# Performance work log

Hardware: AMD Instinct MI355X
Metric: run time of the kernel (lower is better)

## Reference

```python
import jax, jax.numpy as jnp
import numpy as np

C = 512
HEADS = 4
GROUPS = 32
EPS = 1e-6


def setup_inputs() -> dict:
    key = jax.random.key(0)
    ks = jax.random.split(key, 6)
    s = 1.0 / np.sqrt(C)
    return {
        "x": jax.random.normal(ks[0], (2, C, 64, 64), dtype=jnp.float32),
        "gn_scale": jnp.ones((C,), jnp.float32),
        "gn_bias": jnp.zeros((C,), jnp.float32),
        "wq": jax.random.normal(ks[1], (C, C), jnp.float32) * s,
        "bq": jnp.zeros((C,), jnp.float32),
        "wk": jax.random.normal(ks[2], (C, C), jnp.float32) * s,
        "bk": jnp.zeros((C,), jnp.float32),
        "wv": jax.random.normal(ks[3], (C, C), jnp.float32) * s,
        "bv": jnp.zeros((C,), jnp.float32),
        "wo": jax.random.normal(ks[4], (C, C), jnp.float32) * s,
        "bo": jnp.zeros((C,), jnp.float32),
    }


def group_norm(x, scale, bias):
    # x: [b, c, h, w]; GroupNorm with 32 groups, eps 1e-6, affine
    b, c, h, w = x.shape
    xg = x.reshape(b, GROUPS, c // GROUPS, h, w)
    mean = jnp.mean(xg, axis=(2, 3, 4), keepdims=True)
    var = jnp.var(xg, axis=(2, 3, 4), keepdims=True)
    xg = (xg - mean) * jax.lax.rsqrt(var + EPS)
    x = xg.reshape(b, c, h, w)
    return x * scale[None, :, None, None] + bias[None, :, None, None]


def conv1x1(x, w, b):
    # 1x1 conv == per-pixel linear: [b,c,h,w] x [o,c] -> [b,o,h,w]
    return jnp.einsum('bchw,oc->bohw', x, w) + b[None, :, None, None]


def reference(x, gn_scale, gn_bias, wq, bq, wk, bk, wv, bv, wo, bo):
    b, c, h, w = x.shape
    hc = c // HEADS
    n = h * w

    h_ = group_norm(x, gn_scale, gn_bias)
    q = conv1x1(h_, wq, bq).reshape(b, HEADS, hc, n)
    k = conv1x1(h_, wk, bk).reshape(b, HEADS, hc, n)
    v = conv1x1(h_, wv, bv).reshape(b, HEADS, hc, n)

    # NOTE: scale uses full channel count c (repo quirk), not head_channel
    scale = jnp.asarray(c, x.dtype) ** -0.5
    scores = jnp.einsum('bhcn,bhcm->bhnm', q, k) * scale  # [b,H,N,N]
    attn = jax.nn.softmax(scores, axis=-1)
    out = jnp.einsum('bhnm,bhcm->bhcn', attn, v)  # [b,H,hc,N]

    out = out.reshape(b, c, h, w)
    return x + conv1x1(out, wo, bo)
```

## Files before the change

kernel.cpp:

```cpp
#include <hip/hip_runtime.h>

typedef float    f32x4 __attribute__((ext_vector_type(4)));
typedef short    bf16x8 __attribute__((ext_vector_type(8)));
typedef unsigned short u16;
typedef u16      u16x4 __attribute__((ext_vector_type(4)));
typedef unsigned u32;
typedef u32      u32x4 __attribute__((ext_vector_type(4)));

#define MFMA16(a, b, c) __builtin_amdgcn_mfma_f32_16x16x32_bf16((a), (b), (c), 0, 0, 0)

#define CCH 512
#define NPIX 4096
#define NHEAD 4
#define HC 128
#define NSPLIT 2
#define KVCHUNK (NPIX / NSPLIT)
#define QK_SCALE 0.04419417382415922f
#define LOG2E 1.4426950408889634f

__device__ __forceinline__ u16 f2b(float f) {
  unsigned u = __builtin_bit_cast(unsigned, f);
  u += 0x7FFFu + ((u >> 16) & 1u);
  return (u16)(u >> 16);
}
__device__ __forceinline__ float b2f(u16 b) {
  return __builtin_bit_cast(float, ((unsigned)b) << 16);
}

__device__ __forceinline__ void gl_lds16(const u16* g, u16* l) {
  __builtin_amdgcn_global_load_lds((const __attribute__((address_space(1))) void*)g,
                                   (__attribute__((address_space(3))) void*)l, 16, 0, 0);
}

__global__ void prep_k(const float* __restrict__ w0, const float* __restrict__ w1,
                       const float* __restrict__ w2, const float* __restrict__ w3,
                       u16* __restrict__ dst,
                       const float* __restrict__ x, float* __restrict__ pstats) {
  int blk = blockIdx.x, t = threadIdx.x;
  if (blk < 1024) {
    int m = blk >> 8;
    const float* src = (m == 0) ? w0 : (m == 1) ? w1 : (m == 2) ? w2 : w3;
    int i = ((blk & 255) * 256 + t) * 4;
    f32x4 v = *(const f32x4*)(src + i);
    u16x4 o = { f2b(v[0]), f2b(v[1]), f2b(v[2]), f2b(v[3]) };
    *(u16x4*)(dst + (size_t)m * (CCH * CCH) + i) = o;
    return;
  }
  int sblk = blk - 1024;
  const f32x4* p = (const f32x4*)(x + (size_t)sblk * 4096);
  int wv = t >> 6, l = t & 63;
  float s = 0.f, ss = 0.f;
  #pragma unroll
  for (int i = t; i < 1024; i += 256) {
    f32x4 v = p[i];
    s  += v[0] + v[1] + v[2] + v[3];
    ss += v[0]*v[0] + v[1]*v[1] + v[2]*v[2] + v[3]*v[3];
  }
  #pragma unroll
  for (int d = 32; d; d >>= 1) { s += __shfl_down(s, d, 64); ss += __shfl_down(ss, d, 64); }
  __shared__ float red[8];
  if (l == 0) { red[wv*2] = s; red[wv*2+1] = ss; }
  __syncthreads();
  if (t == 0) {
    pstats[sblk*2]   = red[0] + red[2] + red[4] + red[6];
    pstats[sblk*2+1] = red[1] + red[3] + red[5] + red[7];
  }
}

__global__ void gn_norm_k(const float* __restrict__ x, const float* __restrict__ gns,
                          const float* __restrict__ gnb, const float* __restrict__ pstats,
                          u16* __restrict__ Ht) {
  int t = threadIdx.x;
  int ct = blockIdx.x * 64, nt = blockIdx.y * 64, b = blockIdx.z;
  int c0 = ct + (t & 15) * 4;
  int n0 = nt + (t >> 4) * 4;
  const float* xb = x + ((size_t)b * CCH + c0) * NPIX + n0;
  int g = b * 32 + (c0 >> 4);
  const f32x4* ps = (const f32x4*)(pstats + g * 32);
  float s = 0.f, ss = 0.f;
  #pragma unroll
  for (int j = 0; j < 8; ++j) {
    f32x4 v = ps[j];
    s  += v[0] + v[2];
    ss += v[1] + v[3];
  }
  float mean = s * (1.f/65536.f);
  float var  = ss * (1.f/65536.f) - mean*mean;
  float rstd = rsqrtf(var + 1e-6f);
  f32x4 rows[4];
  #pragma unroll
  for (int j = 0; j < 4; ++j) {
    f32x4 v = *(const f32x4*)(xb + (size_t)j * NPIX);
    float a  = rstd * gns[c0 + j];
    float bb = gnb[c0 + j] - mean * a;
    rows[j] = v * a + bb;
  }
  #pragma unroll
  for (int i = 0; i < 4; ++i) {
    u16x4 o = { f2b(rows[0][i]), f2b(rows[1][i]), f2b(rows[2][i]), f2b(rows[3][i]) };
    *(u16x4*)(Ht + ((size_t)b * NPIX + n0 + i) * CCH + c0) = o;
  }
}

template<int MODE>
__device__ __forceinline__ void gemm_body(const u16* __restrict__ A,
                                          const u16* __restrict__ B,
                                          const float* __restrict__ bias,
                                          const float* __restrict__ bias2,
                                          u16* __restrict__ outb,
                                          u16* __restrict__ outb2,
                                          float alpha,
                                          int bx, int by, int z,
                                          u16* As, u16* Bs) {
  const int t = threadIdx.x, l = t & 63, wv = t >> 6;
  const int l16 = l & 15, lq = l >> 4;
  const int mt = bx * 128, nt = by * 64;
  const u16* Ap = A + (size_t)mt * CCH;
  const u16* Bp = (MODE == 3) ? (B + (size_t)nt * CCH)
                              : (B + ((size_t)z * NPIX + nt) * CCH);
  const int wm = (wv >> 1) * 64, wn = (wv & 1) * 32;
  f32x4 acc[4][2] = {};

  #pragma unroll
  for (int j = 0; j < 2; ++j) {
    int idx = t + j * 256;
    int row = idx >> 2, kc = (idx & 3) * 8;
    gl_lds16(Ap + (size_t)row * CCH + kc, As + idx * 8);
  }
  {
    int row = t >> 2, kc = (t & 3) * 8;
    gl_lds16(Bp + (size_t)row * CCH + kc, Bs + t * 8);
  }
  asm volatile("s_waitcnt vmcnt(0)" ::: "memory");
  __syncthreads();

#define GEMM_BODY(CUR, K0, DOSTAGE)                                                   \
  {                                                                                   \
    if (DOSTAGE) {                                                                    \
      _Pragma("unroll")                                                               \
      for (int j = 0; j < 2; ++j) {                                                   \
        int idx = t + j * 256;                                                        \
        int row = idx >> 2, kc = (idx & 3) * 8;                                       \
        gl_lds16(Ap + (size_t)row * CCH + (K0) + 32 + kc, As + ((CUR) ^ 1) * 4096 + idx * 8); \
      }                                                                               \
      {                                                                               \
        int row = t >> 2, kc = (t & 3) * 8;                                           \
        gl_lds16(Bp + (size_t)row * CCH + (K0) + 32 + kc, Bs + ((CUR) ^ 1) * 2048 + t * 8); \
      }                                                                               \
    }                                                                                 \
    bf16x8 af[4], bfr[2];                                                             \
    _Pragma("unroll")                                                                 \
    for (int i = 0; i < 4; ++i)                                                       \
      af[i]  = *(const bf16x8*)(As + (CUR) * 4096 + (wm + i * 16 + l16) * 32 + lq * 8); \
    _Pragma("unroll")                                                                 \
    for (int i = 0; i < 2; ++i)                                                       \
      bfr[i] = *(const bf16x8*)(Bs + (CUR) * 2048 + (wn + i * 16 + l16) * 32 + lq * 8); \
    _Pragma("unroll")                                                                 \
    for (int mi = 0; mi < 4; ++mi)                                                    \
      _Pragma("unroll")                                                               \
      for (int ni = 0; ni < 2; ++ni)                                                  \
        acc[mi][ni] = MFMA16(af[mi], bfr[ni], acc[mi][ni]);                           \
    asm volatile("s_waitcnt vmcnt(0)" ::: "memory");                                  \
    __syncthreads();                                                                  \
  }

  for (int k0 = 0; k0 < CCH; k0 += 64) {
    GEMM_BODY(0, k0, true)
    GEMM_BODY(1, k0 + 32, (k0 + 64 < CCH))
  }
#undef GEMM_BODY

  #pragma unroll
  for (int mi = 0; mi < 4; ++mi)
    #pragma unroll
    for (int ni = 0; ni < 2; ++ni)
      #pragma unroll
      for (int r = 0; r < 4; ++r) {
        int grow = mt + wm + mi * 16 + lq * 4 + r;
        int gcol = nt + wn + ni * 16 + l16;
        float v = acc[mi][ni][r];
        if (MODE == 1) {
          outb[((size_t)z * CCH + grow) * NPIX + gcol] = f2b(v + bias[grow]);
        } else {
          if (gcol < 512)
            outb[(size_t)grow * CCH + gcol] = f2b((v + bias[gcol]) * alpha);
          else
            outb2[(size_t)grow * CCH + (gcol - 512)] = f2b(v + bias2[gcol - 512]);
        }
      }
}

__global__ __launch_bounds__(256) void qkv_k(const u16* __restrict__ Ht,
                                             const u16* __restrict__ wb,
                                             const float* __restrict__ bq,
                                             const float* __restrict__ bk,
                                             const float* __restrict__ bv,
                                             u16* __restrict__ Qt, u16* __restrict__ Kt,
                                             u16* __restrict__ Vc, float alpha) {
  __shared__ __align__(16) u16 As[2][4096];
  __shared__ __align__(16) u16 Bs[2][2048];
  int blk = blockIdx.x;
  if (blk < 1024) {
    gemm_body<3>(Ht, wb, bq, bk, Qt, Kt, alpha, blk >> 4, blk & 15, 0,
                 &As[0][0], &Bs[0][0]);
  } else {
    int r = blk - 1024;
    gemm_body<1>(wb + 2u * 262144u, Ht, bv, nullptr, Vc, nullptr, 1.0f,
                 r & 3, (r >> 2) & 63, r >> 8, &As[0][0], &Bs[0][0]);
  }
}

__global__ __launch_bounds__(256, 2) void flash_k(const u16* __restrict__ Qt,
                                                  const u16* __restrict__ Kt,
                                                  const u16* __restrict__ Vc,
                                                  u16* __restrict__ sl0, u16* __restrict__ sl1,
                                                  float* __restrict__ mlp) {
  __shared__ __align__(16) char lds[32768];
  const int t = threadIdx.x, wv = t >> 6, l = t & 63;
  const int l16 = l & 15, lq = l >> 4;
  const int orig = blockIdx.x;
  const int gid = (orig & 7) * 64 + (orig >> 3);
  const int qx = gid & 31, grp = gid >> 5;
  const int hd = grp & 3, b = (grp >> 2) & 1, s = grp >> 3;
  const int qt0 = qx * 128 + wv * 32;

  const u16* Q = Qt + ((size_t)b * NPIX + qt0) * CCH + hd * HC;
  const u16* Kbase = Kt + (size_t)b * NPIX * CCH + hd * HC;
  const u16* Vbase = Vc + (size_t)b * CCH * NPIX + (size_t)hd * HC * NPIX;
  u16* slab = (s == 0) ? sl0 : sl1;
  u16* Ob = slab + ((size_t)(b * NHEAD + hd) * NPIX + qt0) * HC;
  size_t mlR0 = (size_t)s * 32768 + (size_t)(b * NHEAD + hd) * NPIX + qt0;

  bf16x8 qf[2][4];
  #pragma unroll
  for (int mi = 0; mi < 2; ++mi)
    #pragma unroll
    for (int kk = 0; kk < 4; ++kk)
      qf[mi][kk] = *(const bf16x8*)(Q + (size_t)(mi * 16 + l16) * CCH + kk * 32 + lq * 8);

  const int m_beg = s * KVCHUNK;
  const int vb2 = (lq & 1) * 32 + (lq >> 1) * 16;

  int kbase[4];
  #pragma unroll
  for (int kk = 0; kk < 4; ++kk)
    kbase[kk] = l16 * 256 + ((kk * 64 + lq * 16) ^ ((l16 & 7) << 4));
  const int vbase = 16384 + l16 * 64 + (vb2 ^ ((l16 & 3) << 4));

  u32 kgo[2], vgo[2];
  #pragma unroll
  for (int j = 0; j < 2; ++j) {
    int g = j * 256 + t;
    { int row = g >> 4, src = ((g & 15) << 4) ^ ((row & 7) << 4);
      kgo[j] = (u32)row * CCH + (src >> 1); }
    { int row = g >> 2, src = ((g & 3) << 4) ^ ((row & 3) << 4);
      vgo[j] = (u32)row * NPIX + (src >> 1); }
  }

  const short one_bf = (short)0x3F80;
  const bf16x8 vones = { one_bf, one_bf, one_bf, one_bf, one_bf, one_bf, one_bf, one_bf };

  f32x4 oacc[2][8] = {};
  f32x4 osum[2] = {};

  {
    const u16* kg = Kbase + (size_t)m_beg * CCH;
    const u16* vg = Vbase + m_beg;
    #pragma unroll
    for (int j = 0; j < 2; ++j) {
      gl_lds16(kg + kgo[j], (u16*)lds + (j * 256 + t) * 8);
      gl_lds16(vg + vgo[j], (u16*)(lds + 16384) + (j * 256 + t) * 8);
    }
  }
  asm volatile("s_waitcnt vmcnt(0)" ::: "memory");
  __syncthreads();

  const int NT = KVCHUNK / 32;

#define FLASH_BODY(CUR, M0, DOSTAGE)                                                   \
  {                                                                                    \
    if (DOSTAGE) {                                                                     \
      const u16* kg = Kbase + (size_t)((M0) + 32) * CCH;                               \
      const u16* vg = Vbase + ((M0) + 32);                                             \
      _Pragma("unroll")                                                                \
      for (int j = 0; j < 2; ++j) {                                                    \
        gl_lds16(kg + kgo[j], (u16*)(lds + ((CUR) ^ 1) * 8192) + (j * 256 + t) * 8);   \
        gl_lds16(vg + vgo[j], (u16*)(lds + 16384 + ((CUR) ^ 1) * 8192) + (j * 256 + t) * 8); \
      }                                                                                \
    }                                                                                  \
    f32x4 S[2][2] = {};                                                                \
    __builtin_amdgcn_s_setprio(1);                                                     \
    _Pragma("unroll")                                                                  \
    for (int kk = 0; kk < 4; ++kk)                                                     \
      _Pragma("unroll")                                                                \
      for (int mm = 0; mm < 2; ++mm) {                                                 \
        bf16x8 kf = *(const bf16x8*)(lds + kbase[kk] + mm * 4096 + (CUR) * 8192);      \
        S[0][mm] = MFMA16(kf, qf[0][kk], S[0][mm]);                                    \
        S[1][mm] = MFMA16(kf, qf[1][kk], S[1][mm]);                                    \
      }                                                                                \
    __builtin_amdgcn_s_setprio(0);                                                     \
    u32 pk[2][2][2];                                                                   \
    _Pragma("unroll")                                                                  \
    for (int mi = 0; mi < 2; ++mi) {                                                   \
      _Pragma("unroll")                                                                \
      for (int mm = 0; mm < 2; ++mm) {                                                 \
        f32x4 p;                                                                       \
        _Pragma("unroll")                                                              \
        for (int r = 0; r < 4; ++r) p[r] = exp2f(S[mi][mm][r]);                        \
        asm("v_cvt_pk_bf16_f32 %0, %1, %2" : "=v"(pk[mi][mm][0]) : "v"(p[0]), "v"(p[1])); \
        asm("v_cvt_pk_bf16_f32 %0, %1, %2" : "=v"(pk[mi][mm][1]) : "v"(p[2]), "v"(p[3])); \
      }                                                                                \
    }                                                                                  \
    bf16x8 pa[2];                                                                      \
    _Pragma("unroll")                                                                  \
    for (int mi = 0; mi < 2; ++mi) {                                                   \
      u32 a0 = pk[mi][0][0], a1 = pk[mi][0][1];                                        \
      u32 b0 = pk[mi][1][0], b1 = pk[mi][1][1];                                        \
      asm("v_permlane16_swap_b32 %0, %1" : "+v"(a0), "+v"(b0));                        \
      asm("v_permlane16_swap_b32 %0, %1" : "+v"(a1), "+v"(b1));                        \
      u32x4 w = { a0, a1, b0, b1 };                                                    \
      pa[mi] = __builtin_bit_cast(bf16x8, w);                                          \
    }                                                                                  \
    __builtin_amdgcn_s_setprio(1);                                                     \
    osum[0] = MFMA16(pa[0], vones, osum[0]);                                           \
    osum[1] = MFMA16(pa[1], vones, osum[1]);                                           \
    _Pragma("unroll")                                                                  \
    for (int cc = 0; cc < 8; ++cc) {                                                   \
      bf16x8 vf = *(const bf16x8*)(lds + vbase + cc * 1024 + (CUR) * 8192);            \
      oacc[0][cc] = MFMA16(pa[0], vf, oacc[0][cc]);                                    \
      oacc[1][cc] = MFMA16(pa[1], vf, oacc[1][cc]);                                    \
    }                                                                                  \
    __builtin_amdgcn_s_setprio(0);                                                     \
    asm volatile("s_waitcnt vmcnt(0)" ::: "memory");                                   \
    __syncthreads();                                                                   \
  }

  for (int it = 0; it < NT; it += 2) {
    FLASH_BODY(0, m_beg + it * 32, true)
    FLASH_BODY(1, m_beg + it * 32 + 32, (it + 2 < NT))
  }
#undef FLASH_BODY

  #pragma unroll
  for (int mi = 0; mi < 2; ++mi)
    #pragma unroll
    for (int cc = 0; cc < 8; ++cc)
      #pragma unroll
      for (int r = 0; r < 4; ++r)
        Ob[(size_t)(mi * 16 + lq * 4 + r) * HC + cc * 16 + l16] = f2b(oacc[mi][cc][r]);
  if (l16 == 0) {
    #pragma unroll
    for (int mi = 0; mi < 2; ++mi)
      #pragma unroll
      for (int r = 0; r < 4; ++r)
        mlp[mlR0 + mi * 16 + lq * 4 + r] = osum[mi][r];
  }
}

__global__ __launch_bounds__(256) void fgemm_k(const u16* __restrict__ Wo,
                                               const u16* __restrict__ sl0,
                                               const u16* __restrict__ sl1,
                                               const float* __restrict__ ml,
                                               const float* __restrict__ bias,
                                               const float* __restrict__ resid,
                                               float* __restrict__ outf) {
  __shared__ __align__(16) u16 As[2][4096];
  __shared__ __align__(16) u16 B0[2][2048];
  __shared__ __align__(16) u16 B1[2][2048];
  const int t = threadIdx.x, l = t & 63, wv = t >> 6;
  const int l16 = l & 15, lq = l >> 4;
  const int mt = blockIdx.x * 128, nt = blockIdx.y * 64, z = blockIdx.z;
  const u16* Ap = Wo + (size_t)mt * CCH;
  const int wm = (wv >> 1) * 64, wn = (wv & 1) * 32;

  float lsum[4][2];
  #pragma unroll
  for (int h = 0; h < 4; ++h)
    #pragma unroll
    for (int ni = 0; ni < 2; ++ni) {
      int gcol = nt + wn + ni * 16 + l16;
      int R = ((z * 4 + h) << 12) + gcol;
      lsum[h][ni] = ml[R] + ml[32768 + R];
    }

  f32x4 acc[4][2] = {};

  #pragma unroll
  for (int j = 0; j < 2; ++j) {
    int idx = t + j * 256;
    int row = idx >> 2, kc = (idx & 3) * 8;
    gl_lds16(Ap + (size_t)row * CCH + kc, &As[0][0] + idx * 8);
  }
  {
    int row = t >> 2, kc = (t & 3) * 8;
    size_t srow = ((size_t)(z * 4) * NPIX + nt + row) * HC + kc;
    gl_lds16(sl0 + srow, &B0[0][0] + t * 8);
    gl_lds16(sl1 + srow, &B1[0][0] + t * 8);
  }
  asm volatile("s_waitcnt vmcnt(0)" ::: "memory");
  __syncthreads();

#define FG_BODY(CUR, K0, DOSTAGE)                                                     \
  {                                                                                   \
    if (DOSTAGE) {                                                                    \
      const int kn = (K0) + 32;                                                       \
      const int hn = kn >> 7, cn = kn & 127;                                          \
      _Pragma("unroll")                                                               \
      for (int j = 0; j < 2; ++j) {                                                   \
        int idx = t + j * 256;                                                        \
        int row = idx >> 2, kc = (idx & 3) * 8;                                       \
        gl_lds16(Ap + (size_t)row * CCH + kn + kc, &As[(CUR) ^ 1][0] + idx * 8);      \
      }                                                                               \
      {                                                                               \
        int row = t >> 2, kc = (t & 3) * 8;                                           \
        size_t srow = ((size_t)(z * 4 + hn) * NPIX + nt + row) * HC + cn + kc;        \
        gl_lds16(sl0 + srow, &B0[(CUR) ^ 1][0] + t * 8);                              \
        gl_lds16(sl1 + srow, &B1[(CUR) ^ 1][0] + t * 8);                              \
      }                                                                               \
    }                                                                                 \
    bf16x8 af[4], b0f[2], b1f[2];                                                     \
    _Pragma("unroll")                                                                 \
    for (int i = 0; i < 4; ++i)                                                       \
      af[i]  = *(const bf16x8*)(&As[CUR][0] + (wm + i * 16 + l16) * 32 + lq * 8);     \
    _Pragma("unroll")                                                                 \
    for (int i = 0; i < 2; ++i) {                                                     \
      b0f[i] = *(const bf16x8*)(&B0[CUR][0] + (wn + i * 16 + l16) * 32 + lq * 8);     \
      b1f[i] = *(const bf16x8*)(&B1[CUR][0] + (wn + i * 16 + l16) * 32 + lq * 8);     \
    }                                                                                 \
    _Pragma("unroll")                                                                 \
    for (int mi = 0; mi < 4; ++mi)                                                    \
      _Pragma("unroll")                                                               \
      for (int ni = 0; ni < 2; ++ni) {                                                \
        acc[mi][ni] = MFMA16(af[mi], b0f[ni], acc[mi][ni]);                           \
        acc[mi][ni] = MFMA16(af[mi], b1f[ni], acc[mi][ni]);                           \
      }                                                                               \
    asm volatile("s_waitcnt vmcnt(0)" ::: "memory");                                  \
    __syncthreads();                                                                  \
  }

  #pragma unroll
  for (int h = 0; h < 4; ++h) {
    if (h) {
      #pragma unroll
      for (int ni = 0; ni < 2; ++ni) {
        float rat = lsum[h][ni] / lsum[h - 1][ni];
        #pragma unroll
        for (int mi = 0; mi < 4; ++mi) acc[mi][ni] *= rat;
      }
    }
    FG_BODY(0, h * 128,      true)
    FG_BODY(1, h * 128 + 32, true)
    FG_BODY(0, h * 128 + 64, true)
    FG_BODY(1, h * 128 + 96, (h < 3))
  }
#undef FG_BODY

  #pragma unroll
  for (int ni = 0; ni < 2; ++ni) {
    float inv3 = 1.f / lsum[3][ni];
    int gcol = nt + wn + ni * 16 + l16;
    #pragma unroll
    for (int mi = 0; mi < 4; ++mi)
      #pragma unroll
      for (int r = 0; r < 4; ++r) {
        int grow = mt + wm + mi * 16 + lq * 4 + r;
        size_t off = ((size_t)z * CCH + grow) * NPIX + gcol;
        outf[off] = acc[mi][ni][r] * inv3 + bias[grow] + resid[off];
      }
  }
}

extern "C" void kernel_launch(void* const* d_in, const int* in_sizes, int n_in,
                              void* d_out, int out_size, void* d_ws, size_t ws_size,
                              hipStream_t stream) {
  const float* x   = (const float*)d_in[0];
  const float* gns = (const float*)d_in[1];
  const float* gnb = (const float*)d_in[2];
  const float* wq  = (const float*)d_in[3];
  const float* bq  = (const float*)d_in[4];
  const float* wk  = (const float*)d_in[5];
  const float* bk  = (const float*)d_in[6];
  const float* wv  = (const float*)d_in[7];
  const float* bv  = (const float*)d_in[8];
  const float* wo  = (const float*)d_in[9];
  const float* bo  = (const float*)d_in[10];
  float* out = (float*)d_out;
  char* ws = (char*)d_ws;

  u16*   wb    = (u16*)ws;
  u16*   Ht    = (u16*)(ws + (size_t)( 2u << 20));
  u16*   Qt    = (u16*)(ws + (size_t)(10u << 20));
  u16*   Kt    = (u16*)(ws + (size_t)(18u << 20));
  u16*   Vc    = (u16*)(ws + (size_t)(26u << 20));
  u16*   sl1   = (u16*)(ws + (size_t)(34u << 20));
  float* mlb   = (float*)(ws + (size_t)(42u << 20));
  float* stats = (float*)(ws + (size_t)(43u << 20));
  u16*   sl0   = Ht;

  prep_k    <<<dim3(2048, 1, 1), 256, 0, stream>>>(wq, wk, wv, wo, wb, x, stats);
  gn_norm_k <<<dim3(8, 64, 2),   256, 0, stream>>>(x, gns, gnb, stats, Ht);
  qkv_k     <<<dim3(1536, 1, 1), 256, 0, stream>>>(Ht, wb, bq, bk, bv, Qt, Kt, Vc,
                                                   QK_SCALE * LOG2E);
  flash_k   <<<dim3(512, 1, 1),  256, 0, stream>>>(Qt, Kt, Vc, sl0, sl1, mlb);
  fgemm_k   <<<dim3(4, 64, 2),   256, 0, stream>>>(wb + 3u * 262144u, sl0, sl1, mlb,
                                                   bo, x, out);
}
```

Before: 147.9 us.

## Enlarge QKV GEMM tiles and split flash attention KV range three ways

```diff
diff --git a/kernel.cpp b/kernel.cpp
--- a/kernel.cpp
+++ b/kernel.cpp
@@ -13,8 +13,6 @@
 #define NPIX 4096
 #define NHEAD 4
 #define HC 128
-#define NSPLIT 2
-#define KVCHUNK (NPIX / NSPLIT)
 #define QK_SCALE 0.04419417382415922f
 #define LOG2E 1.4426950408889634f
 
@@ -114,22 +112,19 @@
                                           u16* As, u16* Bs) {
   const int t = threadIdx.x, l = t & 63, wv = t >> 6;
   const int l16 = l & 15, lq = l >> 4;
-  const int mt = bx * 128, nt = by * 64;
+  const int mt = bx * 128, nt = by * 128;
   const u16* Ap = A + (size_t)mt * CCH;
   const u16* Bp = (MODE == 3) ? (B + (size_t)nt * CCH)
                               : (B + ((size_t)z * NPIX + nt) * CCH);
-  const int wm = (wv >> 1) * 64, wn = (wv & 1) * 32;
-  f32x4 acc[4][2] = {};
+  const int wm = (wv >> 1) * 64, wn = (wv & 1) * 64;
+  f32x4 acc[4][4] = {};
 
   #pragma unroll
   for (int j = 0; j < 2; ++j) {
     int idx = t + j * 256;
     int row = idx >> 2, kc = (idx & 3) * 8;
     gl_lds16(Ap + (size_t)row * CCH + kc, As + idx * 8);
-  }
-  {
-    int row = t >> 2, kc = (t & 3) * 8;
-    gl_lds16(Bp + (size_t)row * CCH + kc, Bs + t * 8);
+    gl_lds16(Bp + (size_t)row * CCH + kc, Bs + idx * 8);
   }
   asm volatile("s_waitcnt vmcnt(0)" ::: "memory");
   __syncthreads();
@@ -142,23 +137,19 @@
         int idx = t + j * 256;                                                        \
         int row = idx >> 2, kc = (idx & 3) * 8;                                       \
         gl_lds16(Ap + (size_t)row * CCH + (K0) + 32 + kc, As + ((CUR) ^ 1) * 4096 + idx * 8); \
-      }                                                                               \
-      {                                                                               \
-        int row = t >> 2, kc = (t & 3) * 8;                                           \
-        gl_lds16(Bp + (size_t)row * CCH + (K0) + 32 + kc, Bs + ((CUR) ^ 1) * 2048 + t * 8); \
+        gl_lds16(Bp + (size_t)row * CCH + (K0) + 32 + kc, Bs + ((CUR) ^ 1) * 4096 + idx * 8); \
       }                                                                               \
     }                                                                                 \
-    bf16x8 af[4], bfr[2];                                                             \
+    bf16x8 af[4], bfr[4];                                                             \
     _Pragma("unroll")                                                                 \
-    for (int i = 0; i < 4; ++i)                                                       \
+    for (int i = 0; i < 4; ++i) {                                                     \
       af[i]  = *(const bf16x8*)(As + (CUR) * 4096 + (wm + i * 16 + l16) * 32 + lq * 8); \
-    _Pragma("unroll")                                                                 \
-    for (int i = 0; i < 2; ++i)                                                       \
-      bfr[i] = *(const bf16x8*)(Bs + (CUR) * 2048 + (wn + i * 16 + l16) * 32 + lq * 8); \
+      bfr[i] = *(const bf16x8*)(Bs + (CUR) * 4096 + (wn + i * 16 + l16) * 32 + lq * 8); \
+    }                                                                                 \
     _Pragma("unroll")                                                                 \
     for (int mi = 0; mi < 4; ++mi)                                                    \
       _Pragma("unroll")                                                               \
-      for (int ni = 0; ni < 2; ++ni)                                                  \
+      for (int ni = 0; ni < 4; ++ni)                                                  \
         acc[mi][ni] = MFMA16(af[mi], bfr[ni], acc[mi][ni]);                           \
     asm volatile("s_waitcnt vmcnt(0)" ::: "memory");                                  \
     __syncthreads();                                                                  \
@@ -173,7 +164,7 @@
   #pragma unroll
   for (int mi = 0; mi < 4; ++mi)
     #pragma unroll
-    for (int ni = 0; ni < 2; ++ni)
+    for (int ni = 0; ni < 4; ++ni)
       #pragma unroll
       for (int r = 0; r < 4; ++r) {
         int grow = mt + wm + mi * 16 + lq * 4 + r;
@@ -198,15 +189,15 @@
                                              u16* __restrict__ Qt, u16* __restrict__ Kt,
                                              u16* __restrict__ Vc, float alpha) {
   __shared__ __align__(16) u16 As[2][4096];
-  __shared__ __align__(16) u16 Bs[2][2048];
+  __shared__ __align__(16) u16 Bs[2][4096];
   int blk = blockIdx.x;
-  if (blk < 1024) {
-    gemm_body<3>(Ht, wb, bq, bk, Qt, Kt, alpha, blk >> 4, blk & 15, 0,
+  if (blk < 512) {
+    gemm_body<3>(Ht, wb, bq, bk, Qt, Kt, alpha, blk & 63, blk >> 6, 0,
                  &As[0][0], &Bs[0][0]);
   } else {
-    int r = blk - 1024;
+    int r = blk - 512;
     gemm_body<1>(wb + 2u * 262144u, Ht, bv, nullptr, Vc, nullptr, 1.0f,
-                 r & 3, (r >> 2) & 63, r >> 8, &As[0][0], &Bs[0][0]);
+                 r & 3, (r >> 2) & 31, r >> 7, &As[0][0], &Bs[0][0]);
   }
 }
 
@@ -214,12 +205,13 @@
                                                   const u16* __restrict__ Kt,
                                                   const u16* __restrict__ Vc,
                                                   u16* __restrict__ sl0, u16* __restrict__ sl1,
+                                                  u16* __restrict__ sl2,
                                                   float* __restrict__ mlp) {
   __shared__ __align__(16) char lds[32768];
   const int t = threadIdx.x, wv = t >> 6, l = t & 63;
   const int l16 = l & 15, lq = l >> 4;
   const int orig = blockIdx.x;
-  const int gid = (orig & 7) * 64 + (orig >> 3);
+  const int gid = (orig & 7) * 96 + (orig >> 3);
   const int qx = gid & 31, grp = gid >> 5;
   const int hd = grp & 3, b = (grp >> 2) & 1, s = grp >> 3;
   const int qt0 = qx * 128 + wv * 32;
@@ -227,7 +219,7 @@
   const u16* Q = Qt + ((size_t)b * NPIX + qt0) * CCH + hd * HC;
   const u16* Kbase = Kt + (size_t)b * NPIX * CCH + hd * HC;
   const u16* Vbase = Vc + (size_t)b * CCH * NPIX + (size_t)hd * HC * NPIX;
-  u16* slab = (s == 0) ? sl0 : sl1;
+  u16* slab = (s == 0) ? sl0 : (s == 1) ? sl1 : sl2;
   u16* Ob = slab + ((size_t)(b * NHEAD + hd) * NPIX + qt0) * HC;
   size_t mlR0 = (size_t)s * 32768 + (size_t)(b * NHEAD + hd) * NPIX + qt0;
 
@@ -238,7 +230,8 @@
     for (int kk = 0; kk < 4; ++kk)
       qf[mi][kk] = *(const bf16x8*)(Q + (size_t)(mi * 16 + l16) * CCH + kk * 32 + lq * 8);
 
-  const int m_beg = s * KVCHUNK;
+  const int m_beg = (s == 0) ? 0 : (s == 1) ? 1376 : 2752;
+  const int NT    = (s == 2) ? 42 : 43;
   const int vb2 = (lq & 1) * 32 + (lq >> 1) * 16;
 
   int kbase[4];
@@ -274,8 +267,6 @@
   }
   asm volatile("s_waitcnt vmcnt(0)" ::: "memory");
   __syncthreads();
-
-  const int NT = KVCHUNK / 32;
 
 #define FLASH_BODY(CUR, M0, DOSTAGE)                                                   \
   {                                                                                    \
@@ -335,9 +326,13 @@
     __syncthreads();                                                                   \
   }
 
-  for (int it = 0; it < NT; it += 2) {
+  int it = 0;
+  for (; it + 2 <= NT; it += 2) {
     FLASH_BODY(0, m_beg + it * 32, true)
     FLASH_BODY(1, m_beg + it * 32 + 32, (it + 2 < NT))
+  }
+  if (NT & 1) {
+    FLASH_BODY(0, m_beg + (NT - 1) * 32, false)
   }
 #undef FLASH_BODY
 
@@ -360,6 +355,7 @@
 __global__ __launch_bounds__(256) void fgemm_k(const u16* __restrict__ Wo,
                                                const u16* __restrict__ sl0,
                                                const u16* __restrict__ sl1,
+                                               const u16* __restrict__ sl2,
                                                const float* __restrict__ ml,
                                                const float* __restrict__ bias,
                                                const float* __restrict__ resid,
@@ -367,6 +363,7 @@
   __shared__ __align__(16) u16 As[2][4096];
   __shared__ __align__(16) u16 B0[2][2048];
   __shared__ __align__(16) u16 B1[2][2048];
+  __shared__ __align__(16) u16 B2[2][2048];
   const int t = threadIdx.x, l = t & 63, wv = t >> 6;
   const int l16 = l & 15, lq = l >> 4;
   const int mt = blockIdx.x * 128, nt = blockIdx.y * 64, z = blockIdx.z;
@@ -380,7 +377,7 @@
     for (int ni = 0; ni < 2; ++ni) {
       int gcol = nt + wn + ni * 16 + l16;
       int R = ((z * 4 + h) << 12) + gcol;
-      lsum[h][ni] = ml[R] + ml[32768 + R];
+      lsum[h][ni] = ml[R] + ml[32768 + R] + ml[65536 + R];
     }
 
   f32x4 acc[4][2] = {};
@@ -396,6 +393,7 @@
     size_t srow = ((size_t)(z * 4) * NPIX + nt + row) * HC + kc;
     gl_lds16(sl0 + srow, &B0[0][0] + t * 8);
     gl_lds16(sl1 + srow, &B1[0][0] + t * 8);
+    gl_lds16(sl2 + srow, &B2[0][0] + t * 8);
   }
   asm volatile("s_waitcnt vmcnt(0)" ::: "memory");
   __syncthreads();
@@ -416,23 +414,26 @@
         size_t srow = ((size_t)(z * 4 + hn) * NPIX + nt + row) * HC + cn + kc;        \
         gl_lds16(sl0 + srow, &B0[(CUR) ^ 1][0] + t * 8);                              \
         gl_lds16(sl1 + srow, &B1[(CUR) ^ 1][0] + t * 8);                              \
+        gl_lds16(sl2 + srow, &B2[(CUR) ^ 1][0] + t * 8);                              \
       }                                                                               \
     }                                                                                 \
-    bf16x8 af[4], b0f[2], b1f[2];                                                     \
+    bf16x8 af[4], b0f[2], b1f[2], b2f_[2];                                            \
     _Pragma("unroll")                                                                 \
     for (int i = 0; i < 4; ++i)                                                       \
       af[i]  = *(const bf16x8*)(&As[CUR][0] + (wm + i * 16 + l16) * 32 + lq * 8);     \
     _Pragma("unroll")                                                                 \
     for (int i = 0; i < 2; ++i) {                                                     \
-      b0f[i] = *(const bf16x8*)(&B0[CUR][0] + (wn + i * 16 + l16) * 32 + lq * 8);     \
-      b1f[i] = *(const bf16x8*)(&B1[CUR][0] + (wn + i * 16 + l16) * 32 + lq * 8);     \
+      b0f[i]  = *(const bf16x8*)(&B0[CUR][0] + (wn + i * 16 + l16) * 32 + lq * 8);    \
+      b1f[i]  = *(const bf16x8*)(&B1[CUR][0] + (wn + i * 16 + l16) * 32 + lq * 8);    \
+      b2f_[i] = *(const bf16x8*)(&B2[CUR][0] + (wn + i * 16 + l16) * 32 + lq * 8);    \
     }                                                                                 \
     _Pragma("unroll")                                                                 \
     for (int mi = 0; mi < 4; ++mi)                                                    \
       _Pragma("unroll")                                                               \
       for (int ni = 0; ni < 2; ++ni) {                                                \
-        acc[mi][ni] = MFMA16(af[mi], b0f[ni], acc[mi][ni]);                           \
-        acc[mi][ni] = MFMA16(af[mi], b1f[ni], acc[mi][ni]);                           \
+        acc[mi][ni] = MFMA16(af[mi], b0f[ni],  acc[mi][ni]);                          \
+        acc[mi][ni] = MFMA16(af[mi], b1f[ni],  acc[mi][ni]);                          \
+        acc[mi][ni] = MFMA16(af[mi], b2f_[ni], acc[mi][ni]);                          \
       }                                                                               \
     asm volatile("s_waitcnt vmcnt(0)" ::: "memory");                                  \
     __syncthreads();                                                                  \
@@ -495,13 +496,14 @@
   u16*   sl1   = (u16*)(ws + (size_t)(34u << 20));
   float* mlb   = (float*)(ws + (size_t)(42u << 20));
   float* stats = (float*)(ws + (size_t)(43u << 20));
+  u16*   sl2   = (u16*)(ws + (size_t)(44u << 20));
   u16*   sl0   = Ht;
 
   prep_k    <<<dim3(2048, 1, 1), 256, 0, stream>>>(wq, wk, wv, wo, wb, x, stats);
   gn_norm_k <<<dim3(8, 64, 2),   256, 0, stream>>>(x, gns, gnb, stats, Ht);
-  qkv_k     <<<dim3(1536, 1, 1), 256, 0, stream>>>(Ht, wb, bq, bk, bv, Qt, Kt, Vc,
+  qkv_k     <<<dim3(768, 1, 1),  256, 0, stream>>>(Ht, wb, bq, bk, bv, Qt, Kt, Vc,
                                                    QK_SCALE * LOG2E);
-  flash_k   <<<dim3(512, 1, 1),  256, 0, stream>>>(Qt, Kt, Vc, sl0, sl1, mlb);
-  fgemm_k   <<<dim3(4, 64, 2),   256, 0, stream>>>(wb + 3u * 262144u, sl0, sl1, mlb,
+  flash_k   <<<dim3(768, 1, 1),  256, 0, stream>>>(Qt, Kt, Vc, sl0, sl1, sl2, mlb);
+  fgemm_k   <<<dim3(4, 64, 2),   256, 0, stream>>>(wb + 3u * 262144u, sl0, sl1, sl2, mlb,
                                                    bo, x, out);
 }
```

Measured after the change: 149.5 us. No clear change (+1.1%).
